# Performance work log

Measured on AMD Instinct MI355X. Metric: run time of the kernel, lower is better.

Reference implementation:

```python
import jax, jax.numpy as jnp
import numpy as np

D_MODEL = 2048
D_INNER = 4096
D_STATE = 16
D_CONV = 4
DT_RANK = (D_MODEL + 15) // 16  # 128
BATCH = 2
SEQLEN = 1024


def _silu(x):
    return x * jax.nn.sigmoid(x)


def setup_inputs() -> dict:
    key = jax.random.key(0)
    ks = jax.random.split(key, 9)
    s = 0.02
    # S4D-real style init for A_log so exp(A_log) is well-conditioned
    A_log = jnp.log(jnp.tile(jnp.arange(1, D_STATE + 1, dtype=jnp.float32), (D_INNER, 1)))
    return {
        "index": 0,
        "hidden_states": jax.random.normal(ks[0], (BATCH, SEQLEN, D_MODEL), jnp.float32),
        "in_proj_weight": jax.random.normal(ks[1], (2 * D_INNER, D_MODEL), jnp.float32) * s,
        "conv_weight": jax.random.normal(ks[2], (D_INNER, 1, D_CONV), jnp.float32) * s,
        "conv_bias": jax.random.normal(ks[3], (D_INNER,), jnp.float32) * s,
        "x_proj_weight": jax.random.normal(ks[4], (DT_RANK + 2 * D_STATE, D_INNER), jnp.float32) * s,
        "dt_proj_weight": jax.random.normal(ks[5], (D_INNER, DT_RANK), jnp.float32) * s,
        "dt_proj_bias": jax.random.normal(ks[6], (D_INNER,), jnp.float32) * 0.5,
        "out_proj_weight": jax.random.normal(ks[7], (D_MODEL, D_INNER), jnp.float32) * s,
        "A_log": A_log,
        "D_param": jnp.ones((D_INNER,), jnp.float32),
    }


def _mamba(hidden_states, in_proj_weight, conv_weight, conv_bias, x_proj_weight,
           dt_proj_weight, dt_proj_bias, out_proj_weight, A_log, D_param):
    B, L, _ = hidden_states.shape
    # in_proj: [B, L, 2*d_inner]
    proj = jnp.einsum('bld,ed->ble', hidden_states, in_proj_weight)
    xz = jnp.swapaxes(proj, 1, 2)                      # [B, 2*d_inner, L]
    d_inner = xz.shape[1] // 2
    x, z = xz[:, :d_inner], xz[:, d_inner:]
    # depthwise causal conv1d (torch pads d_conv-1 both sides then truncates to L
    # == left-pad only), then SiLU
    x = jax.lax.conv_general_dilated(
        x, conv_weight, window_strides=(1,), padding=[(conv_weight.shape[-1] - 1, 0)],
        dimension_numbers=('NCH', 'OIH', 'NCH'), feature_group_count=d_inner)
    x = _silu(x + conv_bias[None, :, None])            # [B, d_inner, L]
    # x_proj -> dt, B, C
    x_dbl = jnp.einsum('bdl,ed->bel', x, x_proj_weight)
    dt_rank = dt_proj_weight.shape[1]
    n = A_log.shape[1]
    dt = x_dbl[:, :dt_rank]                            # [B, dt_rank, L]
    Bm = x_dbl[:, dt_rank:dt_rank + n]                 # [B, N, L]
    Cm = x_dbl[:, dt_rank + n:]                        # [B, N, L]
    delta = jnp.einsum('brl,dr->bdl', dt, dt_proj_weight) + dt_proj_bias[None, :, None]
    delta = jax.nn.softplus(delta)                     # delta_softplus=True (bias folded in)
    A = -jnp.exp(A_log.astype(jnp.float32))            # [d_inner, N]

    def step(h, inp):
        d_t, b_t, c_t, u_t = inp                       # [B,d],[B,N],[B,N],[B,d]
        dA = jnp.exp(d_t[..., None] * A)               # [B, d, N]
        h = dA * h + (d_t * u_t)[..., None] * b_t[:, None, :]
        y = jnp.einsum('bdn,bn->bd', h, c_t)
        return h, y

    h0 = jnp.zeros((B, d_inner, n), delta.dtype)
    inps = (jnp.moveaxis(delta, 2, 0), jnp.moveaxis(Bm, 2, 0),
            jnp.moveaxis(Cm, 2, 0), jnp.moveaxis(x, 2, 0))
    _, ys = jax.lax.scan(step, h0, inps)               # [L, B, d_inner]
    y = jnp.moveaxis(ys, 0, 2)                         # [B, d_inner, L]
    y = y + x * D_param[None, :, None]
    y = y * _silu(z)
    out = jnp.einsum('bdl,od->blo', y, out_proj_weight)  # [B, L, d_model]
    return out, proj


def reference(index, hidden_states, in_proj_weight, conv_weight, conv_bias,
              x_proj_weight, dt_proj_weight, dt_proj_bias, out_proj_weight,
              A_log, D_param):
    # `index` is a cache index in the original serving code; unused by the math.
    return _mamba(hidden_states, in_proj_weight, conv_weight, conv_bias,
                  x_proj_weight, dt_proj_weight, dt_proj_bias, out_proj_weight,
                  A_log, D_param)
```

## Files before the change

kernel.cpp:

```cpp
#include <hip/hip_runtime.h>
#include <cstdint>
#include <cstddef>

#define B_  2
#define L_  1024
#define DM  2048
#define DI  4096
#define RR  128
#define UNR 8

using short8 = __attribute__((ext_vector_type(8))) short;
using f32x4  = __attribute__((ext_vector_type(4))) float;

__device__ __forceinline__ float siluf(float v) {
    return v / (1.f + __expf(-v));
}
__device__ __forceinline__ float softplusf(float v) {
    return fmaxf(v, 0.f) + log1pf(__expf(-fabsf(v)));
}
__device__ __forceinline__ unsigned short f2bf(float f) {
    unsigned u = __builtin_bit_cast(unsigned, f);
    u += 0x7fffu + ((u >> 16) & 1u);
    return (unsigned short)(u >> 16);
}

__global__ __launch_bounds__(256)
void cast_bf16_k(const float* __restrict__ s, unsigned short* __restrict__ d, int n8)
{
    const int i = blockIdx.x * 256 + threadIdx.x;
    if (i >= n8) return;
    const float4* sp = (const float4*)s;
    const float4 a = sp[2 * i];
    const float4 b = sp[2 * i + 1];
    short8 o;
    o[0] = (short)f2bf(a.x); o[1] = (short)f2bf(a.y);
    o[2] = (short)f2bf(a.z); o[3] = (short)f2bf(a.w);
    o[4] = (short)f2bf(b.x); o[5] = (short)f2bf(b.y);
    o[6] = (short)f2bf(b.z); o[7] = (short)f2bf(b.w);
    *(short8*)(d + (size_t)i * 8) = o;
}

__global__ __launch_bounds__(256)
void gemm_bf16_mfma(const unsigned short* __restrict__ A16,
                    const unsigned short* __restrict__ B16,
                    float* __restrict__ C, int ldc, int K)
{
    __shared__ unsigned short As[128 * 32];
    __shared__ unsigned short Bs[128 * 32];
    const int t  = threadIdx.x;
    const int w  = t >> 6;
    const int l  = t & 63;
    const int m0 = blockIdx.y * 128;
    const int n0 = blockIdx.x * 128;
    const int wr = w >> 1, wc = w & 1;
    const int lm = l & 15, lk = l >> 4;

    f32x4 acc[4][4] = {};

    for (int k0 = 0; k0 < K; k0 += 32) {
        #pragma unroll
        for (int i = 0; i < 2; ++i) {
            const int cb  = w * 2 + i;
            const int c   = cb * 64 + l;
            const int row = c >> 2, c16 = c & 3;
            const unsigned short* ga = A16 + (size_t)(m0 + row) * K + k0 + c16 * 8;
            const unsigned short* gb = B16 + (size_t)(n0 + row) * K + k0 + c16 * 8;
            __builtin_amdgcn_global_load_lds((const __attribute__((address_space(1))) void*)ga,
                                             (__attribute__((address_space(3))) void*)(As + cb * 512),
                                             16, 0, 0);
            __builtin_amdgcn_global_load_lds((const __attribute__((address_space(1))) void*)gb,
                                             (__attribute__((address_space(3))) void*)(Bs + cb * 512),
                                             16, 0, 0);
        }
        __syncthreads();

        short8 aF[4], bF[4];
        #pragma unroll
        for (int m = 0; m < 4; ++m)
            aF[m] = *(const short8*)(As + (wr * 64 + m * 16 + lm) * 32 + lk * 8);
        #pragma unroll
        for (int n = 0; n < 4; ++n)
            bF[n] = *(const short8*)(Bs + (wc * 64 + n * 16 + lm) * 32 + lk * 8);
        #pragma unroll
        for (int m = 0; m < 4; ++m)
            #pragma unroll
            for (int n = 0; n < 4; ++n)
                acc[m][n] = __builtin_amdgcn_mfma_f32_16x16x32_bf16(aF[m], bF[n], acc[m][n], 0, 0, 0);
        __syncthreads();
    }

    const int cm = m0 + wr * 64 + (l >> 4) * 4;
    const int cn = n0 + wc * 64 + lm;
    #pragma unroll
    for (int m = 0; m < 4; ++m)
        #pragma unroll
        for (int n = 0; n < 4; ++n)
            #pragma unroll
            for (int r = 0; r < 4; ++r)
                C[(size_t)(cm + m * 16 + r) * ldc + cn + n * 16] = acc[m][n][r];
}

template<int EPI>
__global__ __launch_bounds__(256)
void gemm_nt(const float* __restrict__ A, int lda,
             const float* __restrict__ Bw, int ldb,
             float* __restrict__ C, int ldc,
             int N, int K, const float* __restrict__ bias)
{
    __shared__ float As[16][64];
    __shared__ float Bs[16][64];
    const int t  = threadIdx.x;
    const int m0 = blockIdx.y * 64;
    const int n0 = blockIdx.x * 64;
    const int lr = t >> 2;
    const int lc = (t & 3) << 2;
    const int ty = t >> 4;
    const int tx = t & 15;
    float acc[4][4] = {};

    const float* aP = A  + (size_t)(m0 + lr) * lda + lc;
    const float* bP = Bw + (size_t)(n0 + lr) * ldb + lc;
    const bool bok = (n0 + lr) < N;

    for (int k0 = 0; k0 < K; k0 += 16) {
        float4 av = *(const float4*)(aP + k0);
        float4 bv = make_float4(0.f, 0.f, 0.f, 0.f);
        if (bok) bv = *(const float4*)(bP + k0);
        __syncthreads();
        As[lc+0][lr] = av.x; As[lc+1][lr] = av.y; As[lc+2][lr] = av.z; As[lc+3][lr] = av.w;
        Bs[lc+0][lr] = bv.x; Bs[lc+1][lr] = bv.y; Bs[lc+2][lr] = bv.z; Bs[lc+3][lr] = bv.w;
        __syncthreads();
        #pragma unroll
        for (int kk = 0; kk < 16; ++kk) {
            float4 a4 = *(const float4*)&As[kk][ty << 2];
            float4 b4 = *(const float4*)&Bs[kk][tx << 2];
            float a[4] = {a4.x, a4.y, a4.z, a4.w};
            float b[4] = {b4.x, b4.y, b4.z, b4.w};
            #pragma unroll
            for (int i = 0; i < 4; ++i)
                #pragma unroll
                for (int j = 0; j < 4; ++j)
                    acc[i][j] = fmaf(a[i], b[j], acc[i][j]);
        }
    }

    #pragma unroll
    for (int i = 0; i < 4; ++i) {
        const int m = m0 + (ty << 2) + i;
        const int n = n0 + (tx << 2);
        if (n < N) {
            float4 o;
            float* po = (float*)&o;
            #pragma unroll
            for (int j = 0; j < 4; ++j) {
                float v = acc[i][j];
                if (EPI == 1) v = softplusf(v + bias[n + j]);
                po[j] = v;
            }
            *(float4*)(C + (size_t)m * ldc + n) = o;
        }
    }
}

__global__ __launch_bounds__(256)
void gemm_nt_splitk(const float* __restrict__ A, int lda,
                    const float* __restrict__ Bw, int ldb,
                    float* __restrict__ C, int ldc,
                    int N, int Kslice)
{
    __shared__ float As[16][64];
    __shared__ float Bs[16][64];
    const int t  = threadIdx.x;
    const int m0 = blockIdx.y * 64;
    const int n0 = blockIdx.x * 64;
    const int kb = blockIdx.z * Kslice;
    const int lr = t >> 2;
    const int lc = (t & 3) << 2;
    const int ty = t >> 4;
    const int tx = t & 15;
    float acc[4][4] = {};

    const float* aP = A  + (size_t)(m0 + lr) * lda + lc + kb;
    const float* bP = Bw + (size_t)(n0 + lr) * ldb + lc + kb;
    const bool bok = (n0 + lr) < N;

    for (int k0 = 0; k0 < Kslice; k0 += 16) {
        float4 av = *(const float4*)(aP + k0);
        float4 bv = make_float4(0.f, 0.f, 0.f, 0.f);
        if (bok) bv = *(const float4*)(bP + k0);
        __syncthreads();
        As[lc+0][lr] = av.x; As[lc+1][lr] = av.y; As[lc+2][lr] = av.z; As[lc+3][lr] = av.w;
        Bs[lc+0][lr] = bv.x; Bs[lc+1][lr] = bv.y; Bs[lc+2][lr] = bv.z; Bs[lc+3][lr] = bv.w;
        __syncthreads();
        #pragma unroll
        for (int kk = 0; kk < 16; ++kk) {
            float4 a4 = *(const float4*)&As[kk][ty << 2];
            float4 b4 = *(const float4*)&Bs[kk][tx << 2];
            float a[4] = {a4.x, a4.y, a4.z, a4.w};
            float b[4] = {b4.x, b4.y, b4.z, b4.w};
            #pragma unroll
            for (int i = 0; i < 4; ++i)
                #pragma unroll
                for (int j = 0; j < 4; ++j)
                    acc[i][j] = fmaf(a[i], b[j], acc[i][j]);
        }
    }

    #pragma unroll
    for (int i = 0; i < 4; ++i) {
        const int m = m0 + (ty << 2) + i;
        const int n = n0 + (tx << 2);
        if (n < N) {
            #pragma unroll
            for (int j = 0; j < 4; ++j)
                atomicAdd(&C[(size_t)m * ldc + n + j], acc[i][j]);
        }
    }
}

__global__ __launch_bounds__(256)
void conv_silu_k(const float* __restrict__ proj, const float* __restrict__ w,
                 const float* __restrict__ bias, float* __restrict__ xconv)
{
    const int idx = blockIdx.x * 256 + threadIdx.x;
    const int d  = idx & (DI - 1);
    const int bl = idx >> 12;
    const int l  = bl & (L_ - 1);
    const float* pp = proj + (size_t)bl * (2 * DI) + d;
    float acc = bias[d];
    #pragma unroll
    for (int j = 0; j < 4; ++j) {
        const int ls = l - 3 + j;
        if (ls >= 0)
            acc = fmaf(w[(d << 2) + j], pp[(ptrdiff_t)(j - 3) * (2 * DI)], acc);
    }
    xconv[idx] = siluf(acc);
}

__global__ __launch_bounds__(256)
void scan_k(const float* __restrict__ dlt,
            const float* __restrict__ xconv,
            const float* __restrict__ xdbl,
            const float* __restrict__ proj,
            const float* __restrict__ A_log,
            const float* __restrict__ Dp,
            unsigned short* __restrict__ y16)
{
    const int bi = blockIdx.x;
    const int b  = bi >> 8;
    const int t  = threadIdx.x;
    const int n  = t & 15;
    const int d  = ((bi & 255) << 4) + (t >> 4);

    const float An = -__expf(A_log[(d << 4) + n]);
    const float Dd = Dp[d];
    float h = 0.f;

    const float* pd = dlt   + (size_t)(b << 10) * DI + d;
    const float* pu = xconv + (size_t)(b << 10) * DI + d;
    const float* pb = xdbl  + (size_t)(b << 10) * 160 + 128 + n;
    const float* pc = pb + 16;
    const float* pz = proj  + (size_t)(b << 10) * (2 * DI) + DI + d;
    unsigned short* py = y16 + (size_t)(b << 10) * DI + d;

    float dvA[UNR], uuA[UNR], bnA[UNR], cnA[UNR], zzA[UNR];
    float dvB[UNR], uuB[UNR], bnB[UNR], cnB[UNR], zzB[UNR];

#define LOADG(G, L0)                                               \
    { _Pragma("unroll")                                            \
      for (int u = 0; u < UNR; ++u) {                              \
        const int ll = (L0) + u;                                   \
        dv##G[u] = pd[(size_t)ll * DI];                            \
        uu##G[u] = pu[(size_t)ll * DI];                            \
        bn##G[u] = pb[(size_t)ll * 160];                           \
        cn##G[u] = pc[(size_t)ll * 160];                           \
        zz##G[u] = pz[(size_t)ll * (2 * DI)];                      \
      } }

#define COMPG(G, L0)                                               \
    { _Pragma("unroll")                                            \
      for (int u = 0; u < UNR; ++u) {                              \
        const float dA = __expf(dv##G[u] * An);                    \
        h = fmaf(dA, h, dv##G[u] * uu##G[u] * bn##G[u]);           \
        float p = h * cn##G[u];                                    \
        p += __shfl_xor(p, 1);                                     \
        p += __shfl_xor(p, 2);                                     \
        p += __shfl_xor(p, 4);                                     \
        p += __shfl_xor(p, 8);                                     \
        if (n == 0)                                                \
            py[(size_t)((L0) + u) * DI] =                          \
                f2bf((p + uu##G[u] * Dd) * siluf(zz##G[u]));       \
      } }

    LOADG(A, 0)
    for (int l0 = 0; l0 < L_; l0 += 2 * UNR) {
        LOADG(B, l0 + UNR)
        COMPG(A, l0)
        if (l0 + 2 * UNR < L_) LOADG(A, l0 + 2 * UNR)
        COMPG(B, l0 + UNR)
    }
#undef LOADG
#undef COMPG
}

extern "C" void kernel_launch(void* const* d_in, const int* in_sizes, int n_in,
                              void* d_out, int out_size, void* d_ws, size_t ws_size,
                              hipStream_t stream)
{
    const float* hs    = (const float*)d_in[1];
    const float* Win   = (const float*)d_in[2];
    const float* convw = (const float*)d_in[3];
    const float* convb = (const float*)d_in[4];
    const float* Wx    = (const float*)d_in[5];
    const float* Wdt   = (const float*)d_in[6];
    const float* bdt   = (const float*)d_in[7];
    const float* Wout  = (const float*)d_in[8];
    const float* Alog  = (const float*)d_in[9];
    const float* Dp    = (const float*)d_in[10];

    float* out  = (float*)d_out;
    float* proj = out + (size_t)B_ * L_ * DM;

    char* ws = (char*)d_ws;
    unsigned short* Win16  = (unsigned short*)ws;
    float*          xconv  = (float*)ws;
    float*          xdbl   = (float*)(ws + 33554432);
    float*          dlt    = (float*)(ws + 34865152);
    unsigned short* Wout16 = (unsigned short*)(ws + 34865152);
    unsigned short* hs16   = (unsigned short*)(ws + 68419584);
    unsigned short* y16    = (unsigned short*)(ws + 68419584);

    const int M = B_ * L_;

    cast_bf16_k<<<(M * DM / 8 + 255) / 256, 256, 0, stream>>>(hs, hs16, M * DM / 8);
    cast_bf16_k<<<(2 * DI * DM / 8 + 255) / 256, 256, 0, stream>>>(Win, Win16, 2 * DI * DM / 8);

    gemm_bf16_mfma<<<dim3((2 * DI) / 128, M / 128), 256, 0, stream>>>(
        hs16, Win16, proj, 2 * DI, DM);

    conv_silu_k<<<(B_ * L_ * DI) / 256, 256, 0, stream>>>(proj, convw, convb, xconv);

    hipMemsetAsync(xdbl, 0, (size_t)M * 160 * sizeof(float), stream);
    gemm_nt_splitk<<<dim3(3, M / 64, 8), 256, 0, stream>>>(
        xconv, DI, Wx, DI, xdbl, 160, 160, DI / 8);

    gemm_nt<1><<<dim3(DI / 64, M / 64), 256, 0, stream>>>(
        xdbl, 160, Wdt, RR, dlt, DI, DI, RR, bdt);

    scan_k<<<512, 256, 0, stream>>>(dlt, xconv, xdbl, proj, Alog, Dp, y16);

    cast_bf16_k<<<(DM * DI / 8 + 255) / 256, 256, 0, stream>>>(Wout, Wout16, DM * DI / 8);

    gemm_bf16_mfma<<<dim3(DM / 128, M / 128), 256, 0, stream>>>(
        y16, Wout16, out, DM, DI);
}
```

Baseline: 807.3 us.

## Stage scan inputs through double-buffered shared memory with vectorized coalesced loads

The selective-scan kernel now loads 64-step windows of delta, u, B, C and z cooperatively with float4 loads into double-buffered LDS, then runs the recurrence out of shared memory. Previously each thread issued strided scalar global loads per step, and every lane in a 16-lane group redundantly loaded the same per-channel values. The change cuts redundant global traffic and improves coalescing. In exchange it adds LDS usage, a barrier per window, and fewer steps of prefetch lookahead held in registers.

```diff
diff --git a/kernel.cpp b/kernel.cpp
--- a/kernel.cpp
+++ b/kernel.cpp
@@ -7,7 +7,8 @@
 #define DM  2048
 #define DI  4096
 #define RR  128
-#define UNR 8
+#define W_  64
+#define NW  (L_ / W_)
 
 using short8 = __attribute__((ext_vector_type(8))) short;
 using f32x4  = __attribute__((ext_vector_type(4))) float;
@@ -250,57 +251,88 @@
     const int b  = bi >> 8;
     const int t  = threadIdx.x;
     const int n  = t & 15;
-    const int d  = ((bi & 255) << 4) + (t >> 4);
+    const int ch = t >> 4;
+    const int d0 = (bi & 255) << 4;
+    const int d  = d0 + ch;
+
+    __shared__ float dvS[2][W_][16];
+    __shared__ float uuS[2][W_][16];
+    __shared__ float bnS[2][W_][16];
+    __shared__ float cnS[2][W_][16];
+    __shared__ float zzS[2][W_][16];
 
     const float An = -__expf(A_log[(d << 4) + n]);
     const float Dd = Dp[d];
     float h = 0.f;
 
-    const float* pd = dlt   + (size_t)(b << 10) * DI + d;
-    const float* pu = xconv + (size_t)(b << 10) * DI + d;
-    const float* pb = xdbl  + (size_t)(b << 10) * 160 + 128 + n;
-    const float* pc = pb + 16;
-    const float* pz = proj  + (size_t)(b << 10) * (2 * DI) + DI + d;
-    unsigned short* py = y16 + (size_t)(b << 10) * DI + d;
-
-    float dvA[UNR], uuA[UNR], bnA[UNR], cnA[UNR], zzA[UNR];
-    float dvB[UNR], uuB[UNR], bnB[UNR], cnB[UNR], zzB[UNR];
-
-#define LOADG(G, L0)                                               \
-    { _Pragma("unroll")                                            \
-      for (int u = 0; u < UNR; ++u) {                              \
-        const int ll = (L0) + u;                                   \
-        dv##G[u] = pd[(size_t)ll * DI];                            \
-        uu##G[u] = pu[(size_t)ll * DI];                            \
-        bn##G[u] = pb[(size_t)ll * 160];                           \
-        cn##G[u] = pc[(size_t)ll * 160];                           \
-        zz##G[u] = pz[(size_t)ll * (2 * DI)];                      \
-      } }
-
-#define COMPG(G, L0)                                               \
-    { _Pragma("unroll")                                            \
-      for (int u = 0; u < UNR; ++u) {                              \
-        const float dA = __expf(dv##G[u] * An);                    \
-        h = fmaf(dA, h, dv##G[u] * uu##G[u] * bn##G[u]);           \
-        float p = h * cn##G[u];                                    \
-        p += __shfl_xor(p, 1);                                     \
-        p += __shfl_xor(p, 2);                                     \
-        p += __shfl_xor(p, 4);                                     \
-        p += __shfl_xor(p, 8);                                     \
-        if (n == 0)                                                \
-            py[(size_t)((L0) + u) * DI] =                          \
-                f2bf((p + uu##G[u] * Dd) * siluf(zz##G[u]));       \
-      } }
-
-    LOADG(A, 0)
-    for (int l0 = 0; l0 < L_; l0 += 2 * UNR) {
-        LOADG(B, l0 + UNR)
-        COMPG(A, l0)
-        if (l0 + 2 * UNR < L_) LOADG(A, l0 + 2 * UNR)
-        COMPG(B, l0 + UNR)
-    }
-#undef LOADG
-#undef COMPG
+    const int srow = t >> 2;
+    const int sq   = (t & 3) << 2;
+    const size_t bl0 = (size_t)(b << 10);
+
+    const float* gdv = dlt   + (bl0 + srow) * DI + d0 + sq;
+    const float* guu = xconv + (bl0 + srow) * DI + d0 + sq;
+    const float* gbn = xdbl  + (bl0 + srow) * 160 + 128 + sq;
+    const float* gcn = gbn + 16;
+    const float* gzz = proj  + (bl0 + srow) * (2 * DI) + DI + d0 + sq;
+
+    unsigned short* py = y16 + bl0 * DI + d;
+
+    float4 rdv, ruu, rbn, rcn, rzz;
+
+#define LOADW(l0)                                                    \
+    { rdv = *(const float4*)(gdv + (size_t)(l0) * DI);               \
+      ruu = *(const float4*)(guu + (size_t)(l0) * DI);               \
+      rbn = *(const float4*)(gbn + (size_t)(l0) * 160);              \
+      rcn = *(const float4*)(gcn + (size_t)(l0) * 160);              \
+      rzz = *(const float4*)(gzz + (size_t)(l0) * (2 * DI)); }
+
+#define WRITEW(s)                                                    \
+    { *(float4*)&dvS[s][srow][sq] = rdv;                             \
+      *(float4*)&uuS[s][srow][sq] = ruu;                             \
+      *(float4*)&bnS[s][srow][sq] = rbn;                             \
+      *(float4*)&cnS[s][srow][sq] = rcn;                             \
+      *(float4*)&zzS[s][srow][sq] = rzz; }
+
+#define COMPW(s, l0)                                                 \
+    for (int w8 = 0; w8 < W_; w8 += 8) {                             \
+      _Pragma("unroll")                                              \
+      for (int u = 0; u < 8; ++u) {                                  \
+        const int st = w8 + u;                                       \
+        const float dv = dvS[s][st][ch];                             \
+        const float uu = uuS[s][st][ch];                             \
+        const float bn = bnS[s][st][n];                              \
+        const float cn = cnS[s][st][n];                              \
+        const float dA = __expf(dv * An);                            \
+        h = fmaf(dA, h, dv * uu * bn);                               \
+        float p = h * cn;                                            \
+        p += __shfl_xor(p, 1);                                       \
+        p += __shfl_xor(p, 2);                                       \
+        p += __shfl_xor(p, 4);                                       \
+        p += __shfl_xor(p, 8);                                       \
+        if (n == 0) {                                                \
+            const float zz = zzS[s][st][ch];                         \
+            py[(size_t)((l0) + st) * DI] =                           \
+                f2bf((p + uu * Dd) * siluf(zz));                     \
+        }                                                            \
+      }                                                              \
+    }
+
+    LOADW(0);
+    WRITEW(0);
+    __syncthreads();
+    int s = 0;
+    for (int wnd = 0; wnd < NW; ++wnd) {
+        if (wnd + 1 < NW) LOADW((wnd + 1) * W_);
+        COMPW(s, wnd * W_);
+        if (wnd + 1 < NW) {
+            WRITEW(s ^ 1);
+            __syncthreads();
+        }
+        s ^= 1;
+    }
+#undef LOADW
+#undef WRITEW
+#undef COMPW
 }
 
 extern "C" void kernel_launch(void* const* d_in, const int* in_sizes, int n_in,
```

After: 795.6 us. No clear change (-1.5%).
